# Performance work log

Measured on AMD Instinct MI355X. Metric: run time of the kernel, lower is better.

## Reference

```python
import jax, jax.numpy as jnp
import numpy as np

MODEL_DIM = 512
NUM_HEADS = 8
HEAD_DIM = 64
INNER = NUM_HEADS * HEAD_DIM  # 512 == MODEL_DIM -> projection is Identity


def setup_inputs() -> dict:
    key = jax.random.key(0)
    ks = jax.random.split(key, 7)
    B, T = 2, 4096
    x = jax.random.normal(ks[0], (B, T, MODEL_DIM), dtype=jnp.float32)
    s = 1.0 / np.sqrt(MODEL_DIM)
    Wq = jax.random.normal(ks[1], (MODEL_DIM, INNER), dtype=jnp.float32) * s
    Wk = jax.random.normal(ks[2], (MODEL_DIM, INNER), dtype=jnp.float32) * s
    Wv = jax.random.normal(ks[3], (MODEL_DIM, INNER), dtype=jnp.float32) * s
    bq = jax.random.normal(ks[4], (INNER,), dtype=jnp.float32) * 0.01
    bk = jax.random.normal(ks[5], (INNER,), dtype=jnp.float32) * 0.01
    bv = jax.random.normal(ks[6], (INNER,), dtype=jnp.float32) * 0.01
    return {"x": x, "Wq": Wq, "bq": bq, "Wk": Wk, "bk": bk, "Wv": Wv, "bv": bv}


def reference(x, Wq, bq, Wk, bk, Wv, bv):
    B, T, _ = x.shape
    # project and split heads: [B, H, T, D]
    q = (x @ Wq + bq).reshape(B, T, NUM_HEADS, HEAD_DIM).transpose(0, 2, 1, 3)
    k = (x @ Wk + bk).reshape(B, T, NUM_HEADS, HEAD_DIM).transpose(0, 2, 1, 3)
    v = (x @ Wv + bv).reshape(B, T, NUM_HEADS, HEAD_DIM).transpose(0, 2, 1, 3)
    scale = 1.0 / np.sqrt(HEAD_DIM).astype(np.float32)
    attn = jnp.einsum('bhqd,bhkd->bhqk', q, k) * scale  # [B,H,Tq,Tkv]
    attn = jax.nn.softmax(attn, axis=-1)
    out = jnp.einsum('bhqk,bhkd->bhqd', attn, v)        # [B,H,Tq,D]
    out = out.transpose(0, 2, 1, 3).reshape(B, T, INNER)
    return out  # projection is Identity since INNER == MODEL_DIM
```

## Files before the change

kernel.cpp:

```cpp
#include <hip/hip_runtime.h>
#include <hip/hip_bf16.h>


typedef __attribute__((ext_vector_type(8)))  _Float16 half8;
typedef __attribute__((ext_vector_type(2)))  __fp16   fp16x2;
typedef __attribute__((ext_vector_type(4)))  float    f32x4;
typedef __attribute__((ext_vector_type(16))) float    f32x16;

#define TSEQ 4096
#define DH   64
#define NH   8
#define MD   512

#if __has_builtin(__builtin_amdgcn_exp2f)
__device__ inline float fexp2(float x){ return __builtin_amdgcn_exp2f(x); }
#else
__device__ inline float fexp2(float x){ float r; asm("v_exp_f32 %0, %1\n\ts_nop 1" : "=v"(r) : "v"(x)); return r; }
#endif

union H2U { fp16x2 h; unsigned int u; };
__device__ inline unsigned int pkrtz(float a, float b){
  H2U c; c.h = __builtin_amdgcn_cvt_pkrtz(a, b); return c.u;
}

union U4H8 { uint4 u; half8 h; };

#define AS3U(p) ((__attribute__((address_space(3))) unsigned int*)(p))
#define AS1U(p) ((const __attribute__((address_space(1))) unsigned int*)(p))

__global__ __launch_bounds__(256) void k_conv_x(const float* __restrict__ x, _Float16* __restrict__ xh){
  int i = (blockIdx.x*256 + threadIdx.x)*8;
  float4 a = *(const float4*)(x+i);
  float4 b = *(const float4*)(x+i+4);
  half8 o;
  o[0]=(_Float16)a.x; o[1]=(_Float16)a.y; o[2]=(_Float16)a.z; o[3]=(_Float16)a.w;
  o[4]=(_Float16)b.x; o[5]=(_Float16)b.y; o[6]=(_Float16)b.z; o[7]=(_Float16)b.w;
  *(half8*)(xh+i) = o;
}

__global__ __launch_bounds__(256) void k_prep_w(const float* __restrict__ Wq, const float* __restrict__ Wk,
                                                const float* __restrict__ Wv, _Float16* __restrict__ wt){
  __shared__ float tile[32][33];
  const int mat = blockIdx.z;
  const float* W = mat==0 ? Wq : (mat==1 ? Wk : Wv);
  const int n0 = blockIdx.x*32, k0 = blockIdx.y*32;
  const int tx = threadIdx.x & 31, ty = threadIdx.x >> 5;
  #pragma unroll
  for (int i=0;i<4;i++){ int k = ty*4+i; tile[k][tx] = W[(size_t)(k0+k)*MD + n0 + tx]; }
  __syncthreads();
  _Float16* dst = wt + (size_t)mat*MD*MD;
  #pragma unroll
  for (int i=0;i<4;i++){ int n = ty*4+i; dst[(size_t)(n0+n)*MD + k0 + tx] = (_Float16)tile[tx][n]; }
}

__global__ __launch_bounds__(256,2) void k_qkv(const _Float16* __restrict__ xh, const _Float16* __restrict__ wt,
              const float* __restrict__ bq, const float* __restrict__ bk, const float* __restrict__ bv,
              _Float16* __restrict__ qout, _Float16* __restrict__ kout, _Float16* __restrict__ vout){
  __shared__ alignas(16) _Float16 Ash[2][128*64];
  __shared__ alignas(16) _Float16 Bsh[2][128*64];
  const int tid = threadIdx.x, w = tid>>6, l = tid&63;
  const int fr = l&15, hi = l>>4;
  const int nt = blockIdx.x, mt = blockIdx.y;
  const int mat = nt>>2;
  const int n0  = (nt&3)*128;
  const int m0  = mt*128;
  const _Float16* W = wt + (size_t)mat*MD*MD;
  const int wr = (w>>1)*64, wc = (w&1)*64;

  f32x4 acc[4][4];
  #pragma unroll
  for (int a=0;a<4;a++)
    #pragma unroll
    for (int b=0;b<4;b++) acc[a][b] = (f32x4){0.f,0.f,0.f,0.f};

#define QSTAGE(k0_, buf) do { \
    _Pragma("unroll") \
    for (int i_=0;i_<4;i_++){ \
      int slot_ = tid + i_*256; \
      int row_ = slot_>>3, seg_ = (slot_&7) ^ (row_&7); \
      __builtin_amdgcn_global_load_lds(AS1U(xh + (size_t)(m0+row_)*MD + (k0_) + seg_*8), \
          AS3U((char*)&Ash[buf][0] + slot_*16), 16, 0, 0); \
      __builtin_amdgcn_global_load_lds(AS1U(W + (size_t)(n0+row_)*MD + (k0_) + seg_*8), \
          AS3U((char*)&Bsh[buf][0] + slot_*16), 16, 0, 0); \
    } \
  } while(0)

  QSTAGE(0, 0);

  for (int ks0=0; ks0<8; ks0++){
    const int cur = ks0&1;
    __syncthreads();
    if (ks0+1 < 8) QSTAGE((ks0+1)*64, cur^1);
    const _Float16* Ab = &Ash[cur][0];
    const _Float16* Bb = &Bsh[cur][0];
    #pragma unroll
    for (int ks=0;ks<2;ks++){
      half8 af[4], bfr[4];
      #pragma unroll
      for (int mi=0;mi<4;mi++){
        int row = wr + mi*16 + fr;
        af[mi] = *(const half8*)&Ab[row*64 + (((ks*4+hi) ^ (row&7))<<3)];
      }
      #pragma unroll
      for (int ni=0;ni<4;ni++){
        int row = wc + ni*16 + fr;
        bfr[ni] = *(const half8*)&Bb[row*64 + (((ks*4+hi) ^ (row&7))<<3)];
      }
      #pragma unroll
      for (int mi=0;mi<4;mi++)
        #pragma unroll
        for (int ni=0;ni<4;ni++)
          acc[mi][ni] = __builtin_amdgcn_mfma_f32_16x16x32_f16(af[mi], bfr[ni], acc[mi][ni], 0,0,0);
    }
  }
#undef QSTAGE

  const float* bias = mat==0 ? bq : (mat==1 ? bk : bv);
  const float scl = (mat==0) ? 0.125f*1.4426950408889634f : (mat==2 ? 0.0625f : 1.0f);
  if (mat==1){
    #pragma unroll
    for (int ni=0;ni<4;ni++){
      int n_in = n0 + wc + ni*16 + fr;
      float bb = bias[n_in];
      int h = n_in>>6, d = n_in&63;
      #pragma unroll
      for (int mi=0;mi<4;mi++)
        #pragma unroll
        for (int r=0;r<4;r++){
          int m = m0 + wr + mi*16 + hi*4 + r;
          float v = acc[mi][ni][r] + bb;
          int b_ = m>>12, t = m&4095;
          kout[ ((((size_t)(b_*NH + h))*8 + (d>>3))*TSEQ + t)*8 + (d&7) ] = (_Float16)v;
        }
    }
  } else {
    _Float16* dst = mat==0 ? qout : vout;
    #pragma unroll
    for (int ni=0;ni<4;ni++){
      int n_in = n0 + wc + ni*16 + fr;
      float bb = bias[n_in];
      int h = n_in>>6, d = n_in&63;
      #pragma unroll
      for (int mi=0;mi<4;mi++)
        #pragma unroll
        for (int r=0;r<4;r++){
          int m = m0 + wr + mi*16 + hi*4 + r;
          float v = (acc[mi][ni][r] + bb)*scl;
          int b_ = m>>12, t = m&4095;
          dst[ ((size_t)((b_*NH + h)*TSEQ + t))*DH + d ] = (_Float16)v;
        }
    }
  }
}

__global__ __launch_bounds__(256) void k_trans_v(const _Float16* __restrict__ v, _Float16* __restrict__ vtg){
  __shared__ _Float16 tile[64][72];
  const int tid = threadIdx.x;
  const int bh = blockIdx.y, t0 = blockIdx.x*64;
  const _Float16* src = v + ((size_t)bh*TSEQ + t0)*DH;
  #pragma unroll
  for (int i=0;i<2;i++){
    int slot = tid + i*256; int r = slot>>3, s = slot&7;
    *(half8*)&tile[r][s*8] = *(const half8*)(src + (size_t)r*DH + s*8);
  }
  __syncthreads();
  #pragma unroll
  for (int i=0;i<2;i++){
    int slot = tid + i*256;
    int d = slot&63, sg = slot>>6;
    half8 o;
    #pragma unroll
    for (int j=0;j<8;j++) o[j] = tile[sg*8+j][d];
    *(half8*)(vtg + (((size_t)bh*512 + (t0>>3) + sg)*64 + d)*8) = o;
  }
}

__global__ __launch_bounds__(256,2) void k_attn(const _Float16* __restrict__ qb_, const _Float16* __restrict__ ktg,
                                                const _Float16* __restrict__ vtg, float* __restrict__ out){
  __shared__ alignas(16) _Float16 Ksh[2*8192];
  __shared__ alignas(16) _Float16 Vsh[2*8192];
  const int tid = threadIdx.x, w = tid>>6, l = tid&63;
  const int ln31 = l&31, lh = l>>5;

  const int bid = blockIdx.x;
  const int swz = ((bid&7)<<6) | (bid>>3);
  const int bh = swz>>5, qblk = swz&31;

  const _Float16* Q  = qb_ + (size_t)bh*TSEQ*DH;
  const _Float16* Kt = ktg + (size_t)bh*8*TSEQ*8;
  const _Float16* Vt = vtg + (size_t)bh*512*64*8;
  const int q0 = qblk*128 + w*32;

  half8 qf[4];
  #pragma unroll
  for (int ds=0;ds<4;ds++)
    qf[ds] = *(const half8*)(Q + (size_t)(q0 + ln31)*DH + ds*16 + lh*8);

  f32x16 of0, of1, sacc;
  #pragma unroll
  for (int r=0;r<16;r++){ of0[r]=0.f; of1[r]=0.f; sacc[r]=0.f; }
  const half8 onesv = {(_Float16)1,(_Float16)1,(_Float16)1,(_Float16)1,
                       (_Float16)1,(_Float16)1,(_Float16)1,(_Float16)1};

  const int NT = TSEQ/128;
  const int kbase = lh*1024 + ln31*8;
  const int vbase = lh*512  + ln31*8;

#define STAGE(kt, buf) do { \
    const int k0_ = (kt)*128; \
    _Pragma("unroll") \
    for (int i_=0;i_<4;i_++){ \
      int base_ = i_*256 + w*64; \
      int slot_ = base_ + l; \
      int krow_ = slot_&127, kseg_ = slot_>>7; \
      __builtin_amdgcn_global_load_lds(AS1U(Kt + ((size_t)kseg_*TSEQ + k0_ + krow_)*8), \
          AS3U((char*)Ksh + (buf)*16384 + base_*16), 16, 0, 0); \
      __builtin_amdgcn_global_load_lds(AS1U(Vt + ((size_t)slot_ + k0_*8)*8), \
          AS3U((char*)Vsh + (buf)*16384 + base_*16), 16, 0, 0); \
    } \
  } while(0)

  STAGE(0, 0);

  for (int kt=0; kt<NT; kt++){
    const int cur = kt&1;
    __syncthreads();
    if (kt+1 < NT) STAGE(kt+1, cur^1);

    const _Float16* Kb = &Ksh[cur*8192];
    const _Float16* Vb = &Vsh[cur*8192];

    #pragma unroll
    for (int kbq=0; kbq<4; kbq++){
      f32x16 s;
      #pragma unroll
      for (int r=0;r<16;r++) s[r]=0.f;
      __builtin_amdgcn_s_setprio(1);
      #pragma unroll
      for (int ds=0;ds<4;ds++){
        half8 kf = *(const half8*)&Kb[kbase + ds*2048 + kbq*256];
        s = __builtin_amdgcn_mfma_f32_32x32x16_f16(kf, qf[ds], s, 0,0,0);
      }
      __builtin_amdgcn_s_setprio(0);

      unsigned int wv[8];
      #pragma unroll
      for (int c=0;c<4;c++){
        float e0 = fexp2(s[4*c+0]);
        float e1 = fexp2(s[4*c+1]);
        float e2 = fexp2(s[4*c+2]);
        float e3 = fexp2(s[4*c+3]);
        wv[2*c+0] = pkrtz(e0, e1);
        wv[2*c+1] = pkrtz(e2, e3);
      }

      #pragma unroll
      for (int e=0;e<2;e++){
        unsigned int word[4];
        #pragma unroll
        for (int i=0;i<2;i++){
          unsigned int w0 = wv[4*e + i];
          unsigned int w1 = wv[4*e + 2 + i];
          unsigned int exp_ = (lh==0) ? w1 : w0;
          unsigned int cross = (unsigned int)__shfl((int)exp_, l ^ 32);
          word[i]   = (lh==0) ? w0 : cross;
          word[2+i] = (lh==0) ? cross : w1;
        }
        U4H8 pf; pf.u.x=word[0]; pf.u.y=word[1]; pf.u.z=word[2]; pf.u.w=word[3];
        half8 v0 = *(const half8*)&Vb[vbase + kbq*2048 + e*1024];
        half8 v1 = *(const half8*)&Vb[vbase + kbq*2048 + e*1024 + 256];
        __builtin_amdgcn_s_setprio(1);
        sacc = __builtin_amdgcn_mfma_f32_32x32x16_f16(onesv, pf.h, sacc, 0,0,0);
        of0 = __builtin_amdgcn_mfma_f32_32x32x16_f16(v0, pf.h, of0, 0,0,0);
        of1 = __builtin_amdgcn_mfma_f32_32x32x16_f16(v1, pf.h, of1, 0,0,0);
        __builtin_amdgcn_s_setprio(0);
      }
    }
  }

  float inv = 16.0f / sacc[0];

  const int b_ = bh>>3, h = bh&7;
  float* o = out + ((size_t)(b_*TSEQ + q0 + ln31))*MD + h*DH;
  #pragma unroll
  for (int rr=0;rr<4;rr++){
    float4 o4 = { of0[4*rr+0]*inv, of0[4*rr+1]*inv, of0[4*rr+2]*inv, of0[4*rr+3]*inv };
    *(float4*)(o + rr*8 + lh*4) = o4;
  }
  #pragma unroll
  for (int rr=0;rr<4;rr++){
    float4 o4 = { of1[4*rr+0]*inv, of1[4*rr+1]*inv, of1[4*rr+2]*inv, of1[4*rr+3]*inv };
    *(float4*)(o + 32 + rr*8 + lh*4) = o4;
  }
#undef STAGE
}

extern "C" void kernel_launch(void* const* d_in, const int* in_sizes, int n_in,
                              void* d_out, int out_size, void* d_ws, size_t ws_size,
                              hipStream_t stream) {
  const float* x  = (const float*)d_in[0];
  const float* Wq = (const float*)d_in[1];
  const float* bq = (const float*)d_in[2];
  const float* Wk = (const float*)d_in[3];
  const float* bk = (const float*)d_in[4];
  const float* Wv = (const float*)d_in[5];
  const float* bv = (const float*)d_in[6];
  float* out = (float*)d_out;

  char* ws = (char*)d_ws;
  _Float16* xh = (_Float16*)(ws);
  _Float16* wt = (_Float16*)(ws + ((size_t)8<<20));
  _Float16* qb = (_Float16*)(ws + ((size_t)10<<20));
  _Float16* kb = (_Float16*)(ws + ((size_t)18<<20));
  _Float16* vb = (_Float16*)(ws + ((size_t)26<<20));
  _Float16* vt = xh;

  k_conv_x<<<2048, 256, 0, stream>>>(x, xh);
  k_prep_w<<<dim3(16,16,3), 256, 0, stream>>>(Wq, Wk, Wv, wt);
  k_qkv<<<dim3(12,64), 256, 0, stream>>>(xh, wt, bq, bk, bv, qb, kb, vb);
  k_trans_v<<<dim3(64,16), 256, 0, stream>>>(vb, vt);
  k_attn<<<512, 256, 0, stream>>>(qb, kb, vt, out);
}
```

Before: 139.6 us.

## Split attention KV range across two blocks and combine partials in a new kernel

Splits each query block's key/value sequence into two halves handled by separate blocks, doubling the grid to 1024 blocks. LDS tiles shrink to 64 keys and launch bounds rise to 4 blocks per CU, aiming for higher occupancy and better CU fill. Since softmax is computed without a running max, the partials add directly: one half writes to out, the other to an fp16 buffer, and row sums go to a separate buffer. A new combine kernel adds them and normalizes, which costs extra global traffic, an extra launch, and fp16 rounding on half the partial output. The setprio hints were also removed.

```diff
diff --git a/kernel.cpp b/kernel.cpp
--- a/kernel.cpp
+++ b/kernel.cpp
@@ -175,16 +175,19 @@
   }
 }
 
-__global__ __launch_bounds__(256,2) void k_attn(const _Float16* __restrict__ qb_, const _Float16* __restrict__ ktg,
-                                                const _Float16* __restrict__ vtg, float* __restrict__ out){
-  __shared__ alignas(16) _Float16 Ksh[2*8192];
-  __shared__ alignas(16) _Float16 Vsh[2*8192];
+__global__ __launch_bounds__(256,4) void k_attn(const _Float16* __restrict__ qb_, const _Float16* __restrict__ ktg,
+                                                const _Float16* __restrict__ vtg, float* __restrict__ out,
+                                                _Float16* __restrict__ pb, float* __restrict__ ps){
+  __shared__ alignas(16) _Float16 Ksh[2*4096];
+  __shared__ alignas(16) _Float16 Vsh[2*4096];
   const int tid = threadIdx.x, w = tid>>6, l = tid&63;
   const int ln31 = l&31, lh = l>>5;
 
   const int bid = blockIdx.x;
-  const int swz = ((bid&7)<<6) | (bid>>3);
-  const int bh = swz>>5, qblk = swz&31;
+  const int swz = ((bid&7)<<7) | (bid>>3);
+  const int bh = swz>>6;
+  const int qblk = (swz&63)>>1;
+  const int half = swz&1;
 
   const _Float16* Q  = qb_ + (size_t)bh*TSEQ*DH;
   const _Float16* Kt = ktg + (size_t)bh*8*TSEQ*8;
@@ -202,46 +205,43 @@
   const half8 onesv = {(_Float16)1,(_Float16)1,(_Float16)1,(_Float16)1,
                        (_Float16)1,(_Float16)1,(_Float16)1,(_Float16)1};
 
-  const int NT = TSEQ/128;
-  const int kbase = lh*1024 + ln31*8;
-  const int vbase = lh*512  + ln31*8;
+  const int base16 = lh*512 + ln31*8;
 
 #define STAGE(kt, buf) do { \
-    const int k0_ = (kt)*128; \
+    const int k0_ = (kt)*64; \
     _Pragma("unroll") \
-    for (int i_=0;i_<4;i_++){ \
+    for (int i_=0;i_<2;i_++){ \
       int base_ = i_*256 + w*64; \
       int slot_ = base_ + l; \
-      int krow_ = slot_&127, kseg_ = slot_>>7; \
+      int krow_ = slot_&63, kseg_ = slot_>>6; \
       __builtin_amdgcn_global_load_lds(AS1U(Kt + ((size_t)kseg_*TSEQ + k0_ + krow_)*8), \
-          AS3U((char*)Ksh + (buf)*16384 + base_*16), 16, 0, 0); \
-      __builtin_amdgcn_global_load_lds(AS1U(Vt + ((size_t)slot_ + k0_*8)*8), \
-          AS3U((char*)Vsh + (buf)*16384 + base_*16), 16, 0, 0); \
+          AS3U((char*)Ksh + (buf)*8192 + base_*16), 16, 0, 0); \
+      __builtin_amdgcn_global_load_lds(AS1U(Vt + ((size_t)(slot_ + k0_*8))*8), \
+          AS3U((char*)Vsh + (buf)*8192 + base_*16), 16, 0, 0); \
     } \
   } while(0)
 
-  STAGE(0, 0);
-
-  for (int kt=0; kt<NT; kt++){
-    const int cur = kt&1;
+  const int kt0 = half*32;
+  STAGE(kt0, 0);
+
+  for (int it=0; it<32; it++){
+    const int cur = it&1;
     __syncthreads();
-    if (kt+1 < NT) STAGE(kt+1, cur^1);
-
-    const _Float16* Kb = &Ksh[cur*8192];
-    const _Float16* Vb = &Vsh[cur*8192];
-
-    #pragma unroll
-    for (int kbq=0; kbq<4; kbq++){
+    if (it+1 < 32) STAGE(kt0+it+1, cur^1);
+
+    const _Float16* Kb = &Ksh[cur*4096];
+    const _Float16* Vb = &Vsh[cur*4096];
+
+    #pragma unroll
+    for (int kbq=0; kbq<2; kbq++){
       f32x16 s;
       #pragma unroll
       for (int r=0;r<16;r++) s[r]=0.f;
-      __builtin_amdgcn_s_setprio(1);
       #pragma unroll
       for (int ds=0;ds<4;ds++){
-        half8 kf = *(const half8*)&Kb[kbase + ds*2048 + kbq*256];
+        half8 kf = *(const half8*)&Kb[base16 + ds*1024 + kbq*256];
         s = __builtin_amdgcn_mfma_f32_32x32x16_f16(kf, qf[ds], s, 0,0,0);
       }
-      __builtin_amdgcn_s_setprio(0);
 
       unsigned int wv[8];
       #pragma unroll
@@ -267,32 +267,62 @@
           word[2+i] = (lh==0) ? cross : w1;
         }
         U4H8 pf; pf.u.x=word[0]; pf.u.y=word[1]; pf.u.z=word[2]; pf.u.w=word[3];
-        half8 v0 = *(const half8*)&Vb[vbase + kbq*2048 + e*1024];
-        half8 v1 = *(const half8*)&Vb[vbase + kbq*2048 + e*1024 + 256];
-        __builtin_amdgcn_s_setprio(1);
+        const int ea = kbq*2 + e;
+        half8 v0 = *(const half8*)&Vb[base16 + ea*1024];
+        half8 v1 = *(const half8*)&Vb[base16 + ea*1024 + 256];
         sacc = __builtin_amdgcn_mfma_f32_32x32x16_f16(onesv, pf.h, sacc, 0,0,0);
         of0 = __builtin_amdgcn_mfma_f32_32x32x16_f16(v0, pf.h, of0, 0,0,0);
         of1 = __builtin_amdgcn_mfma_f32_32x32x16_f16(v1, pf.h, of1, 0,0,0);
-        __builtin_amdgcn_s_setprio(0);
-      }
-    }
-  }
-
-  float inv = 16.0f / sacc[0];
-
-  const int b_ = bh>>3, h = bh&7;
-  float* o = out + ((size_t)(b_*TSEQ + q0 + ln31))*MD + h*DH;
-  #pragma unroll
-  for (int rr=0;rr<4;rr++){
-    float4 o4 = { of0[4*rr+0]*inv, of0[4*rr+1]*inv, of0[4*rr+2]*inv, of0[4*rr+3]*inv };
-    *(float4*)(o + rr*8 + lh*4) = o4;
-  }
-  #pragma unroll
-  for (int rr=0;rr<4;rr++){
-    float4 o4 = { of1[4*rr+0]*inv, of1[4*rr+1]*inv, of1[4*rr+2]*inv, of1[4*rr+3]*inv };
-    *(float4*)(o + 32 + rr*8 + lh*4) = o4;
+      }
+    }
+  }
+
+  if (lh==0) ps[half*65536 + bh*TSEQ + q0 + ln31] = sacc[0];
+
+  if (half==0){
+    const int b_ = bh>>3, h = bh&7;
+    float* o = out + ((size_t)(b_*TSEQ + q0 + ln31))*MD + h*DH;
+    #pragma unroll
+    for (int rr=0;rr<4;rr++){
+      float4 o4 = { of0[4*rr+0], of0[4*rr+1], of0[4*rr+2], of0[4*rr+3] };
+      *(float4*)(o + rr*8 + lh*4) = o4;
+    }
+    #pragma unroll
+    for (int rr=0;rr<4;rr++){
+      float4 o4 = { of1[4*rr+0], of1[4*rr+1], of1[4*rr+2], of1[4*rr+3] };
+      *(float4*)(o + 32 + rr*8 + lh*4) = o4;
+    }
+  } else {
+    _Float16* o = pb + ((size_t)bh*TSEQ + q0 + ln31)*DH;
+    #pragma unroll
+    for (int rr=0;rr<4;rr++){
+      uint2 pk = { pkrtz(of0[4*rr+0], of0[4*rr+1]), pkrtz(of0[4*rr+2], of0[4*rr+3]) };
+      *(uint2*)(o + rr*8 + lh*4) = pk;
+    }
+    #pragma unroll
+    for (int rr=0;rr<4;rr++){
+      uint2 pk = { pkrtz(of1[4*rr+0], of1[4*rr+1]), pkrtz(of1[4*rr+2], of1[4*rr+3]) };
+      *(uint2*)(o + 32 + rr*8 + lh*4) = pk;
+    }
   }
 #undef STAGE
+}
+
+__global__ __launch_bounds__(256) void k_comb(float* __restrict__ out, const _Float16* __restrict__ pb,
+                                              const float* __restrict__ ps){
+  int idx = (blockIdx.x*256 + threadIdx.x)*8;
+  int d0 = idx & 511, t = (idx>>9)&4095, b = idx>>21;
+  int h = d0>>6, bh = b*NH + h;
+  float sc = 16.0f / (ps[bh*TSEQ + t] + ps[65536 + bh*TSEQ + t]);
+  float4 a0 = *(float4*)(out+idx);
+  float4 a1 = *(float4*)(out+idx+4);
+  half8 pv = *(const half8*)(pb + ((size_t)bh*TSEQ + t)*DH + (d0&63));
+  float4 r0 = { (a0.x + (float)pv[0])*sc, (a0.y + (float)pv[1])*sc,
+                (a0.z + (float)pv[2])*sc, (a0.w + (float)pv[3])*sc };
+  float4 r1 = { (a1.x + (float)pv[4])*sc, (a1.y + (float)pv[5])*sc,
+                (a1.z + (float)pv[6])*sc, (a1.w + (float)pv[7])*sc };
+  *(float4*)(out+idx)   = r0;
+  *(float4*)(out+idx+4) = r1;
 }
 
 extern "C" void kernel_launch(void* const* d_in, const int* in_sizes, int n_in,
@@ -314,10 +344,13 @@
   _Float16* kb = (_Float16*)(ws + ((size_t)18<<20));
   _Float16* vb = (_Float16*)(ws + ((size_t)26<<20));
   _Float16* vt = xh;
+  _Float16* pb = vb;
+  float*    ps = (float*)(ws + ((size_t)8<<20));
 
   k_conv_x<<<2048, 256, 0, stream>>>(x, xh);
   k_prep_w<<<dim3(16,16,3), 256, 0, stream>>>(Wq, Wk, Wv, wt);
   k_qkv<<<dim3(12,64), 256, 0, stream>>>(xh, wt, bq, bk, bv, qb, kb, vb);
   k_trans_v<<<dim3(64,16), 256, 0, stream>>>(vb, vt);
-  k_attn<<<512, 256, 0, stream>>>(qb, kb, vt, out);
-}
+  k_attn<<<1024, 256, 0, stream>>>(qb, kb, vt, out, pb, ps);
+  k_comb<<<2048, 256, 0, stream>>>(out, pb, ps);
+}
```

Measured after the change: 139.4 us. Within noise of the previous version (-0.2%).
